# Kernel optimization log

Hardware: AMD Instinct MI355X
Metric: run time of the kernel (lower is better)

Reference implementation:

```python
import jax, jax.numpy as jnp
import numpy as np
from jax import lax

N = 25600      # total nodes = G * T
E = 204800     # edges (before self loops)
IN_CH = 6
HID = 64
HEADS = 4
G = 512        # graphs per batch
T = 50         # sequence length (node_time in [0, T))
OUT = 30       # prediction_horizon * 3
NEG_SLOPE = 0.2
BN_EPS = 1e-5


def _gat(x, src, dst, W, a_src, a_dst, b, heads, outc):
    # PyG GATConv (concat=True): h = x W reshaped to (N, H, C)
    n = x.shape[0]
    h = (x @ W).reshape(n, heads, outc)
    # edge scores: leaky_relu(a_src . h_src + a_dst . h_dst), softmax over incoming edges of dst
    e = jax.nn.leaky_relu((h * a_src).sum(-1)[src] + (h * a_dst).sum(-1)[dst], NEG_SLOPE)  # (E, H)
    m = jax.ops.segment_max(e, dst, num_segments=n)
    ex = jnp.exp(e - m[dst])
    denom = jax.ops.segment_sum(ex, dst, num_segments=n)
    alpha = ex / denom[dst]
    out = jax.ops.segment_sum(alpha[:, :, None] * h[src], dst, num_segments=n)  # (N, H, C)
    return out.reshape(n, heads * outc) + b


def _bn_eval(x, g, b):
    # BatchNorm in eval with running_mean=0, running_var=1
    return g * (x * (1.0 / np.float32(np.sqrt(1.0 + BN_EPS)))) + b


def setup_inputs() -> dict:
    ks = jax.random.split(jax.random.key(0), 16)
    s = 0.1
    d = {}
    d["x"] = jax.random.normal(ks[0], (N, IN_CH), jnp.float32)
    d["edge_index"] = jax.random.randint(ks[1], (2, E), 0, N)
    idx = jnp.arange(N)
    d["batch"] = idx // T       # each graph has exactly T nodes
    d["node_time"] = idx % T
    d["W1"] = jax.random.normal(ks[2], (IN_CH, HEADS * HID), jnp.float32) * s
    d["att_src1"] = jax.random.normal(ks[3], (HEADS, HID), jnp.float32) * s
    d["att_dst1"] = jax.random.normal(ks[4], (HEADS, HID), jnp.float32) * s
    d["b1"] = jnp.zeros((HEADS * HID,), jnp.float32)
    d["g1"] = jnp.ones((HEADS * HID,), jnp.float32)
    d["be1"] = jnp.zeros((HEADS * HID,), jnp.float32)
    d["W2"] = jax.random.normal(ks[5], (HEADS * HID, HID), jnp.float32) * s
    d["att_src2"] = jax.random.normal(ks[6], (1, HID), jnp.float32) * s
    d["att_dst2"] = jax.random.normal(ks[7], (1, HID), jnp.float32) * s
    d["b2"] = jnp.zeros((HID,), jnp.float32)
    d["g2"] = jnp.ones((HID,), jnp.float32)
    d["be2"] = jnp.zeros((HID,), jnp.float32)
    d["Wih"] = jax.random.normal(ks[8], (4 * HID, HID), jnp.float32) * s
    d["Whh"] = jax.random.normal(ks[9], (4 * HID, HID), jnp.float32) * s
    d["bih"] = jnp.zeros((4 * HID,), jnp.float32)
    d["bhh"] = jnp.zeros((4 * HID,), jnp.float32)
    d["Wfc"] = jax.random.normal(ks[10], (HID, OUT), jnp.float32) * s
    d["bfc"] = jnp.zeros((OUT,), jnp.float32)
    return d


def reference(x, edge_index, batch, node_time, W1, att_src1, att_dst1, b1, g1, be1,
              W2, att_src2, att_dst2, b2, g2, be2, Wih, Whh, bih, bhh, Wfc, bfc):
    loops = jnp.arange(N)
    src = jnp.concatenate([edge_index[0], loops])  # GATConv adds self loops
    dst = jnp.concatenate([edge_index[1], loops])
    h = jax.nn.elu(_bn_eval(_gat(x, src, dst, W1, att_src1, att_dst1, b1, HEADS, HID), g1, be1))
    h = jax.nn.elu(_bn_eval(_gat(h, src, dst, W2, att_src2, att_dst2, b2, 1, HID), g2, be2))
    # vectorized replacement of the per-node python scatter loop
    x_seq = jnp.zeros((G, T, HID), h.dtype).at[batch, node_time].set(h)

    def step(carry, xt):
        hh, cc = carry
        gates = xt @ Wih.T + bih + hh @ Whh.T + bhh
        i, f, gg, o = jnp.split(gates, 4, axis=-1)
        cc = jax.nn.sigmoid(f) * cc + jax.nn.sigmoid(i) * jnp.tanh(gg)
        hh = jax.nn.sigmoid(o) * jnp.tanh(cc)
        return (hh, cc), None

    init = (jnp.zeros((G, HID), h.dtype), jnp.zeros((G, HID), h.dtype))
    (hn, _), _ = lax.scan(step, init, x_seq.transpose(1, 0, 2))  # scan over time
    return hn @ Wfc + bfc  # (G, 30)
```

## Files before the change

### kernel.cpp

```cpp
#include <hip/hip_runtime.h>

#define N_NODES 25600
#define N_EDGES 204800
#define EE (N_EDGES + N_NODES)
#define IN_CH 6
#define HID 64
#define HEADS 4
#define G_GRAPHS 512
#define T_STEPS 50
#define OUT_DIM 30
#define NEG_SLOPE 0.2f
#define BN_INV 0.9999950000374997f

__device__ __forceinline__ float lrelu_(float x){ return x > 0.f ? x : NEG_SLOPE * x; }
__device__ __forceinline__ float elu_(float x){ return x > 0.f ? x : __expf(x) - 1.f; }
__device__ __forceinline__ float sigmoid_(float x){
    return __builtin_amdgcn_rcpf(1.f + __expf(-x));
}
__device__ __forceinline__ float tanh_(float x){
    return 1.f - 2.f * __builtin_amdgcn_rcpf(1.f + __expf(2.f * x));
}

__global__ void count_k(const int* __restrict__ ei, int* __restrict__ counts){
    int e = blockIdx.x * 256 + threadIdx.x;
    if (e >= EE) return;
    int dst = (e < N_EDGES) ? ei[N_EDGES + e] : (e - N_EDGES);
    atomicAdd(&counts[dst], 1);
}

__global__ void scan_k(const int* __restrict__ counts, int* __restrict__ row_ptr,
                       int* __restrict__ cursor){
    __shared__ int part[1024];
    int t = threadIdx.x;
    const int CH = N_NODES / 1024;
    int base = t * CH;
    int s = 0;
    for (int i = 0; i < CH; i++) s += counts[base + i];
    part[t] = s;
    __syncthreads();
    for (int off = 1; off < 1024; off <<= 1){
        int v = (t >= off) ? part[t - off] : 0;
        __syncthreads();
        part[t] += v;
        __syncthreads();
    }
    int run = (t > 0) ? part[t - 1] : 0;
    for (int i = 0; i < CH; i++){
        int cv = counts[base + i];
        row_ptr[base + i] = run;
        cursor[base + i]  = run;
        run += cv;
    }
    if (t == 1023) row_ptr[N_NODES] = run;
}

__global__ void scatter_k(const int* __restrict__ ei, int* __restrict__ cursor,
                          int* __restrict__ ssrc){
    int e = blockIdx.x * 256 + threadIdx.x;
    if (e >= EE) return;
    int src, dst;
    if (e < N_EDGES){ src = ei[e]; dst = ei[N_EDGES + e]; }
    else            { src = dst = e - N_EDGES; }
    int pos = atomicAdd(&cursor[dst], 1);
    ssrc[pos] = src;
}

__global__ void ns_k(const float* __restrict__ x, const float* __restrict__ W1,
                     const float* __restrict__ asw, const float* __restrict__ adw,
                     float* __restrict__ as1, float* __restrict__ ad1){
    __shared__ float waS[IN_CH * 4], waD[IN_CH * 4];
    int t = threadIdx.x;
    if (t < 48){
        int k = t >> 3, h = (t >> 1) & 3, which = t & 1;
        const float* a = which ? adw : asw;
        float s = 0.f;
        #pragma unroll
        for (int c = 0; c < 64; c++) s += W1[k * 256 + h * 64 + c] * a[h * 64 + c];
        (which ? waD : waS)[k * 4 + h] = s;
    }
    __syncthreads();
    int n = blockIdx.x * 256 + t;
    float xv[IN_CH];
    #pragma unroll
    for (int k = 0; k < IN_CH; k++) xv[k] = x[n * IN_CH + k];
    float sv[4] = {0.f, 0.f, 0.f, 0.f}, dv[4] = {0.f, 0.f, 0.f, 0.f};
    #pragma unroll
    for (int k = 0; k < IN_CH; k++){
        #pragma unroll
        for (int h = 0; h < 4; h++){
            sv[h] += xv[k] * waS[k * 4 + h];
            dv[h] += xv[k] * waD[k * 4 + h];
        }
    }
    *(float4*)&as1[n * 4] = make_float4(sv[0], sv[1], sv[2], sv[3]);
    *(float4*)&ad1[n * 4] = make_float4(dv[0], dv[1], dv[2], dv[3]);
}

__global__ void gat1_aggx(const float* __restrict__ x, const float* __restrict__ as1,
                          const float* __restrict__ ad1, const int* __restrict__ row_ptr,
                          const int* __restrict__ ssrc, const float* __restrict__ W1,
                          const float* __restrict__ b1, const float* __restrict__ g1,
                          const float* __restrict__ be1, float* __restrict__ h1_act){
    __shared__ float w1s[IN_CH * 256];
    int tid = threadIdx.x;
    for (int i = tid; i < IN_CH * 256; i += 256) w1s[i] = W1[i];
    __syncthreads();
    int wv = tid >> 6, lane = tid & 63;
    int n = blockIdx.x * 4 + wv;
    int s0 = row_ptr[n], s1 = row_ptr[n + 1];
    float4 adn = *(const float4*)&ad1[n * 4];
    float xs0[IN_CH] = {}, xs1[IN_CH] = {}, xs2[IN_CH] = {}, xs3[IN_CH] = {};
    float d0 = 0.f, d1 = 0.f, d2 = 0.f, d3 = 0.f;
    for (int j = s0; j < s1; j++){
        int s = ssrc[j];
        float4 as = *(const float4*)&as1[s * 4];
        float e0 = __expf(lrelu_(as.x + adn.x));
        float e1 = __expf(lrelu_(as.y + adn.y));
        float e2 = __expf(lrelu_(as.z + adn.z));
        float e3 = __expf(lrelu_(as.w + adn.w));
        d0 += e0; d1 += e1; d2 += e2; d3 += e3;
        const float2* xp = (const float2*)(x + (size_t)s * IN_CH);
        float2 xa = xp[0], xb = xp[1], xc = xp[2];
        float xv[IN_CH] = {xa.x, xa.y, xb.x, xb.y, xc.x, xc.y};
        #pragma unroll
        for (int k = 0; k < IN_CH; k++){
            xs0[k] += e0 * xv[k];
            xs1[k] += e1 * xv[k];
            xs2[k] += e2 * xv[k];
            xs3[k] += e3 * xv[k];
        }
    }
    float r0 = 1.f / d0, r1 = 1.f / d1, r2 = 1.f / d2, r3 = 1.f / d3;
    #pragma unroll
    for (int h = 0; h < 4; h++){
        const float* xsh = (h == 0) ? xs0 : (h == 1) ? xs1 : (h == 2) ? xs2 : xs3;
        float rh = (h == 0) ? r0 : (h == 1) ? r1 : (h == 2) ? r2 : r3;
        int col = h * 64 + lane;
        float acc = 0.f;
        #pragma unroll
        for (int k = 0; k < IN_CH; k++) acc += xsh[k] * w1s[k * 256 + col];
        float v = acc * rh + b1[col];
        v = g1[col] * (v * BN_INV) + be1[col];
        h1_act[(size_t)n * 256 + col] = elu_(v);
    }
}

#define TM 64
#define KT 32
#define APAD 4
__global__ __launch_bounds__(256) void gat2_tr(const float* __restrict__ h1_act,
                        const float* __restrict__ W2,
                        const float* __restrict__ asw, const float* __restrict__ adw,
                        float* __restrict__ h2_pre, float* __restrict__ as2,
                        float* __restrict__ ad2){
    __shared__ float As[TM][KT + APAD];
    __shared__ float Bs[KT][64];
    int tx = threadIdx.x;
    int rg = tx >> 4;
    int cg = tx & 15;
    int r0 = rg * 4, c0 = cg * 4;
    int rowBase = blockIdx.x * TM;
    float acc[4][4] = {};
    for (int k0 = 0; k0 < 256; k0 += KT){
        #pragma unroll
        for (int it = 0; it < 2; it++){
            int i = tx + it * 256;
            int row = i >> 3;
            int c4  = (i & 7) * 4;
            *(float4*)&As[row][c4] =
                *(const float4*)(h1_act + (size_t)(rowBase + row) * 256 + k0 + c4);
        }
        #pragma unroll
        for (int it = 0; it < 2; it++){
            int i = tx + it * 256;
            int row = i >> 4;
            int c4  = (i & 15) * 4;
            *(float4*)&Bs[row][c4] = *(const float4*)(W2 + (size_t)(k0 + row) * 64 + c4);
        }
        __syncthreads();
        #pragma unroll
        for (int kq = 0; kq < KT; kq += 4){
            float4 b0 = *(float4*)&Bs[kq + 0][c0];
            float4 b1v = *(float4*)&Bs[kq + 1][c0];
            float4 b2v = *(float4*)&Bs[kq + 2][c0];
            float4 b3 = *(float4*)&Bs[kq + 3][c0];
            #pragma unroll
            for (int i = 0; i < 4; i++){
                float4 a = *(float4*)&As[r0 + i][kq];
                acc[i][0] += a.x * b0.x + a.y * b1v.x + a.z * b2v.x + a.w * b3.x;
                acc[i][1] += a.x * b0.y + a.y * b1v.y + a.z * b2v.y + a.w * b3.y;
                acc[i][2] += a.x * b0.z + a.y * b1v.z + a.z * b2v.z + a.w * b3.z;
                acc[i][3] += a.x * b0.w + a.y * b1v.w + a.z * b2v.w + a.w * b3.w;
            }
        }
        __syncthreads();
    }
    float aw0 = asw[c0], aw1 = asw[c0+1], aw2 = asw[c0+2], aw3 = asw[c0+3];
    float dw0 = adw[c0], dw1 = adw[c0+1], dw2 = adw[c0+2], dw3 = adw[c0+3];
    #pragma unroll
    for (int i = 0; i < 4; i++){
        int row = rowBase + r0 + i;
        *(float4*)(h2_pre + (size_t)row * 64 + c0) =
            make_float4(acc[i][0], acc[i][1], acc[i][2], acc[i][3]);
        float sA = acc[i][0]*aw0 + acc[i][1]*aw1 + acc[i][2]*aw2 + acc[i][3]*aw3;
        float sD = acc[i][0]*dw0 + acc[i][1]*dw1 + acc[i][2]*dw2 + acc[i][3]*dw3;
        #pragma unroll
        for (int off = 8; off; off >>= 1){
            sA += __shfl_xor(sA, off);
            sD += __shfl_xor(sD, off);
        }
        if (cg == 0){ as2[row] = sA; ad2[row] = sD; }
    }
}

__global__ __launch_bounds__(256, 2) void gat2_aggp(const float* __restrict__ h2_pre,
        const float* __restrict__ as2, const float* __restrict__ ad2,
        const int* __restrict__ row_ptr, const int* __restrict__ ssrc,
        const float* __restrict__ b2, const float* __restrict__ g2,
        const float* __restrict__ be2,
        const int* __restrict__ batch, const int* __restrict__ ntime,
        const float* __restrict__ Wih, const float* __restrict__ bih,
        const float* __restrict__ bhh, float* __restrict__ gx){
    __shared__ float vsh[16][64];
    __shared__ int posb[16];
    int tx = threadIdx.x, wv = tx >> 6, lane = tx & 63;
    float4 wih[16];
    const float4* Wr = (const float4*)(Wih + tx * 64);
    #pragma unroll
    for (int k = 0; k < 16; k++) wih[k] = Wr[k];
    float bsum = bih[tx] + bhh[tx];
    int nbase = blockIdx.x * 16;
    for (int q = 0; q < 4; q++){
        int n = nbase + wv * 4 + q;
        int s0 = row_ptr[n], s1 = row_ptr[n + 1];
        float adn = ad2[n];
        float denom = 0.f, acc = 0.f;
        int j = s0;
        for (; j + 4 <= s1; j += 4){
            int sa = ssrc[j], sb = ssrc[j + 1], sc = ssrc[j + 2], sd = ssrc[j + 3];
            float ea = __expf(lrelu_(as2[sa] + adn));
            float eb = __expf(lrelu_(as2[sb] + adn));
            float ec = __expf(lrelu_(as2[sc] + adn));
            float ed = __expf(lrelu_(as2[sd] + adn));
            float ha = h2_pre[(size_t)sa * 64 + lane];
            float hb = h2_pre[(size_t)sb * 64 + lane];
            float hc = h2_pre[(size_t)sc * 64 + lane];
            float hd = h2_pre[(size_t)sd * 64 + lane];
            denom += (ea + eb) + (ec + ed);
            acc += ea * ha + eb * hb + ec * hc + ed * hd;
        }
        for (; j < s1; j++){
            int s = ssrc[j];
            float e = __expf(lrelu_(as2[s] + adn));
            denom += e;
            acc += e * h2_pre[(size_t)s * 64 + lane];
        }
        float v = acc / denom + b2[lane];
        v = g2[lane] * (v * BN_INV) + be2[lane];
        vsh[wv * 4 + q][lane] = elu_(v);
        if (lane == 0) posb[wv * 4 + q] = batch[n] * T_STEPS + ntime[n];
    }
    __syncthreads();
    #pragma unroll
    for (int q = 0; q < 16; q++){
        const float4* vp = (const float4*)vsh[q];
        float a0 = 0.f, a1 = 0.f, a2 = 0.f, a3 = 0.f;
        #pragma unroll
        for (int k = 0; k < 16; k++){
            float4 vv = vp[k];
            float4 ww = wih[k];
            a0 += ww.x * vv.x;
            a1 += ww.y * vv.y;
            a2 += ww.z * vv.z;
            a3 += ww.w * vv.w;
        }
        gx[(size_t)posb[q] * 256 + tx] = bsum + (a0 + a1) + (a2 + a3);
    }
}

__global__ __launch_bounds__(256, 2) void lstm_k(const float* __restrict__ gx,
        const float* __restrict__ Whh,
        const float* __restrict__ Wfc, const float* __restrict__ bfc,
        float* __restrict__ out){
    int g = blockIdx.x;
    int j = threadIdx.x;
    int wv = j >> 6, lane = j & 63;
    __shared__ float gates[2][256];
    __shared__ float hb[4][2][64];
    float4 whh[16];
    const float4* Hr = (const float4*)(Whh + j * 64);
    #pragma unroll
    for (int k = 0; k < 16; k++) whh[k] = Hr[k];
    float c = 0.f;
    hb[wv][0][lane] = 0.f;
    const float* gxg = gx + (size_t)g * T_STEPS * 256;
    float gxv = gxg[j];
    float hn = 0.f;
    for (int t = 0; t < T_STEPS; t++){
        float gx_next = (t + 1 < T_STEPS) ? gxg[(t + 1) * 256 + j] : 0.f;
        int buf = t & 1;
        const float4* hp = (const float4*)hb[wv][buf];
        float a0 = gxv, a1 = 0.f, a2 = 0.f, a3 = 0.f;
        #pragma unroll
        for (int k = 0; k < 16; k++){
            float4 hv = hp[k];
            float4 wvv = whh[k];
            a0 += wvv.x * hv.x;
            a1 += wvv.y * hv.y;
            a2 += wvv.z * hv.z;
            a3 += wvv.w * hv.w;
        }
        gates[buf][j] = (a0 + a1) + (a2 + a3);
        __syncthreads();
        float iv = gates[buf][lane];
        float fv = gates[buf][64 + lane];
        float gv = gates[buf][128 + lane];
        float ov = gates[buf][192 + lane];
        c = sigmoid_(fv) * c + sigmoid_(iv) * tanh_(gv);
        hn = sigmoid_(ov) * tanh_(c);
        hb[wv][buf ^ 1][lane] = hn;
        gxv = gx_next;
    }
    if (wv == 0) gates[0][lane] = hn;
    __syncthreads();
    if (j < OUT_DIM){
        float acc = bfc[j];
        #pragma unroll
        for (int k = 0; k < 64; k++) acc += gates[0][k] * Wfc[k * OUT_DIM + j];
        out[g * OUT_DIM + j] = acc;
    }
}

extern "C" void kernel_launch(void* const* d_in, const int* in_sizes, int n_in,
                              void* d_out, int out_size, void* d_ws, size_t ws_size,
                              hipStream_t stream){
    const float* x    = (const float*)d_in[0];
    const int*   ei   = (const int*)  d_in[1];
    const int*   batch= (const int*)  d_in[2];
    const int*   ntime= (const int*)  d_in[3];
    const float* W1   = (const float*)d_in[4];
    const float* as1w = (const float*)d_in[5];
    const float* ad1w = (const float*)d_in[6];
    const float* b1   = (const float*)d_in[7];
    const float* g1   = (const float*)d_in[8];
    const float* be1  = (const float*)d_in[9];
    const float* W2   = (const float*)d_in[10];
    const float* as2w = (const float*)d_in[11];
    const float* ad2w = (const float*)d_in[12];
    const float* b2   = (const float*)d_in[13];
    const float* g2   = (const float*)d_in[14];
    const float* be2  = (const float*)d_in[15];
    const float* Wih  = (const float*)d_in[16];
    const float* Whh  = (const float*)d_in[17];
    const float* bih  = (const float*)d_in[18];
    const float* bhh  = (const float*)d_in[19];
    const float* Wfc  = (const float*)d_in[20];
    const float* bfc  = (const float*)d_in[21];
    float* out = (float*)d_out;

    char* w = (char*)d_ws;
    auto alloc = [&](size_t bytes)->char*{
        char* p = w;
        w += (bytes + 255) & ~size_t(255);
        return p;
    };
    float* h1_act = (float*)alloc((size_t)N_NODES * 256 * 4);
    float* gx     = (float*)alloc((size_t)N_NODES * 256 * 4);
    float* h2_pre = (float*)alloc((size_t)N_NODES * 64 * 4);
    float* as1    = (float*)alloc((size_t)N_NODES * 4 * 4);
    float* ad1    = (float*)alloc((size_t)N_NODES * 4 * 4);
    float* as2    = (float*)alloc((size_t)N_NODES * 4);
    float* ad2    = (float*)alloc((size_t)N_NODES * 4);
    int* counts   = (int*)alloc((size_t)N_NODES * 4);
    int* row_ptr  = (int*)alloc((size_t)(N_NODES + 1) * 4);
    int* cursor   = (int*)alloc((size_t)N_NODES * 4);
    int* ssrc     = (int*)alloc((size_t)EE * 4);

    hipMemsetAsync(counts, 0, (size_t)N_NODES * 4, stream);
    count_k  <<<(EE + 255) / 256, 256, 0, stream>>>(ei, counts);
    scan_k   <<<1, 1024, 0, stream>>>(counts, row_ptr, cursor);
    scatter_k<<<(EE + 255) / 256, 256, 0, stream>>>(ei, cursor, ssrc);
    ns_k     <<<N_NODES / 256, 256, 0, stream>>>(x, W1, as1w, ad1w, as1, ad1);
    gat1_aggx<<<N_NODES / 4, 256, 0, stream>>>(x, as1, ad1, row_ptr, ssrc, W1, b1, g1, be1, h1_act);
    gat2_tr  <<<N_NODES / TM, 256, 0, stream>>>(h1_act, W2, as2w, ad2w, h2_pre, as2, ad2);
    gat2_aggp<<<N_NODES / 16, 256, 0, stream>>>(h2_pre, as2, ad2, row_ptr, ssrc, b2, g2, be2,
                                                batch, ntime, Wih, bih, bhh, gx);
    lstm_k   <<<G_GRAPHS, 256, 0, stream>>>(gx, Whh, Wfc, bfc, out);
}
```

Baseline: 291.4 us.

## Use lane broadcasts for input projection and LSTM recurrence, two graphs per block

Adds a kernel that transposes Wih so the gate-projection epilogue in gat2_aggp streams coalesced weight rows and broadcasts node features via readlane, instead of holding 64 weights per thread in registers. The LSTM kernel now runs two graphs per 512-thread block, broadcasts the hidden state across lanes with readlane instead of a shared-memory buffer, and reloads Whh rows from memory each step rather than keeping them in registers. The aim is lower register pressure and higher occupancy. The cost is an extra launch and more global/L1 traffic for weights. Within each wavefront all 64 hidden values are available, so the lane broadcast is correct.

```diff
diff --git a/kernel.cpp b/kernel.cpp
--- a/kernel.cpp
+++ b/kernel.cpp
@@ -20,6 +20,9 @@
 __device__ __forceinline__ float tanh_(float x){
     return 1.f - 2.f * __builtin_amdgcn_rcpf(1.f + __expf(2.f * x));
 }
+__device__ __forceinline__ float bcast_(float v, int l){
+    return __int_as_float(__builtin_amdgcn_readlane(__float_as_int(v), l));
+}
 
 __global__ void count_k(const int* __restrict__ ei, int* __restrict__ counts){
     int e = blockIdx.x * 256 + threadIdx.x;
@@ -63,6 +66,21 @@
     else            { src = dst = e - N_EDGES; }
     int pos = atomicAdd(&cursor[dst], 1);
     ssrc[pos] = src;
+}
+
+__global__ void twih_k(const float* __restrict__ Wih, float* __restrict__ WihT){
+    __shared__ float tile[64][65];
+    int t = threadIdx.x;
+    int jb = blockIdx.x * 64;
+    for (int i = t; i < 64 * 64; i += 256){
+        int j = i >> 6, k = i & 63;
+        tile[k][j] = Wih[(size_t)(jb + j) * 64 + k];
+    }
+    __syncthreads();
+    for (int i = t; i < 64 * 64; i += 256){
+        int k = i >> 6, j = i & 63;
+        WihT[(size_t)k * 256 + jb + j] = tile[k][j];
+    }
 }
 
 __global__ void ns_k(const float* __restrict__ x, const float* __restrict__ W1,
@@ -219,16 +237,11 @@
         const float* __restrict__ b2, const float* __restrict__ g2,
         const float* __restrict__ be2,
         const int* __restrict__ batch, const int* __restrict__ ntime,
-        const float* __restrict__ Wih, const float* __restrict__ bih,
+        const float* __restrict__ WihT, const float* __restrict__ bih,
         const float* __restrict__ bhh, float* __restrict__ gx){
     __shared__ float vsh[16][64];
     __shared__ int posb[16];
     int tx = threadIdx.x, wv = tx >> 6, lane = tx & 63;
-    float4 wih[16];
-    const float4* Wr = (const float4*)(Wih + tx * 64);
-    #pragma unroll
-    for (int k = 0; k < 16; k++) wih[k] = Wr[k];
-    float bsum = bih[tx] + bhh[tx];
     int nbase = blockIdx.x * 16;
     for (int q = 0; q < 4; q++){
         int n = nbase + wv * 4 + q;
@@ -261,73 +274,65 @@
         if (lane == 0) posb[wv * 4 + q] = batch[n] * T_STEPS + ntime[n];
     }
     __syncthreads();
-    #pragma unroll
-    for (int q = 0; q < 16; q++){
-        const float4* vp = (const float4*)vsh[q];
-        float a0 = 0.f, a1 = 0.f, a2 = 0.f, a3 = 0.f;
-        #pragma unroll
-        for (int k = 0; k < 16; k++){
-            float4 vv = vp[k];
-            float4 ww = wih[k];
-            a0 += ww.x * vv.x;
-            a1 += ww.y * vv.y;
-            a2 += ww.z * vv.z;
-            a3 += ww.w * vv.w;
-        }
-        gx[(size_t)posb[q] * 256 + tx] = bsum + (a0 + a1) + (a2 + a3);
-    }
-}
-
-__global__ __launch_bounds__(256, 2) void lstm_k(const float* __restrict__ gx,
+    float vq[16];
+    #pragma unroll
+    for (int q = 0; q < 16; q++) vq[q] = vsh[q][lane];
+    float bsum = bih[tx] + bhh[tx];
+    float acc[16];
+    #pragma unroll
+    for (int q = 0; q < 16; q++) acc[q] = bsum;
+    #pragma unroll 4
+    for (int k = 0; k < 64; k++){
+        float wk = WihT[(size_t)k * 256 + tx];
+        #pragma unroll
+        for (int q = 0; q < 16; q++)
+            acc[q] += wk * bcast_(vq[q], k);
+    }
+    #pragma unroll
+    for (int q = 0; q < 16; q++)
+        gx[(size_t)posb[q] * 256 + tx] = acc[q];
+}
+
+__global__ __launch_bounds__(512, 2) void lstm_k(const float* __restrict__ gx,
         const float* __restrict__ Whh,
         const float* __restrict__ Wfc, const float* __restrict__ bfc,
         float* __restrict__ out){
-    int g = blockIdx.x;
-    int j = threadIdx.x;
-    int wv = j >> 6, lane = j & 63;
-    __shared__ float gates[2][256];
-    __shared__ float hb[4][2][64];
-    float4 whh[16];
-    const float4* Hr = (const float4*)(Whh + j * 64);
-    #pragma unroll
-    for (int k = 0; k < 16; k++) whh[k] = Hr[k];
-    float c = 0.f;
-    hb[wv][0][lane] = 0.f;
-    const float* gxg = gx + (size_t)g * T_STEPS * 256;
-    float gxv = gxg[j];
-    float hn = 0.f;
+    int g0 = blockIdx.x * 2;
+    int t0 = threadIdx.x;
+    int gr = t0 >> 8;
+    int j  = t0 & 255;
+    int lane = t0 & 63;
+    __shared__ float gates[2][2][256];
+    const float4* Wr = (const float4*)(Whh + (size_t)j * 64);
+    const float* gxg = gx + (size_t)(g0 + gr) * T_STEPS * 256 + j;
+    float c = 0.f, hn = 0.f;
     for (int t = 0; t < T_STEPS; t++){
-        float gx_next = (t + 1 < T_STEPS) ? gxg[(t + 1) * 256 + j] : 0.f;
         int buf = t & 1;
-        const float4* hp = (const float4*)hb[wv][buf];
-        float a0 = gxv, a1 = 0.f, a2 = 0.f, a3 = 0.f;
+        float a0 = gxg[t * 256], a1 = 0.f, a2 = 0.f, a3 = 0.f;
         #pragma unroll
         for (int k = 0; k < 16; k++){
-            float4 hv = hp[k];
-            float4 wvv = whh[k];
-            a0 += wvv.x * hv.x;
-            a1 += wvv.y * hv.y;
-            a2 += wvv.z * hv.z;
-            a3 += wvv.w * hv.w;
-        }
-        gates[buf][j] = (a0 + a1) + (a2 + a3);
-        __syncthreads();
-        float iv = gates[buf][lane];
-        float fv = gates[buf][64 + lane];
-        float gv = gates[buf][128 + lane];
-        float ov = gates[buf][192 + lane];
+            float4 wv = Wr[k];
+            a0 += wv.x * bcast_(hn, 4 * k + 0);
+            a1 += wv.y * bcast_(hn, 4 * k + 1);
+            a2 += wv.z * bcast_(hn, 4 * k + 2);
+            a3 += wv.w * bcast_(hn, 4 * k + 3);
+        }
+        gates[gr][buf][j] = (a0 + a1) + (a2 + a3);
+        __syncthreads();
+        float iv = gates[gr][buf][lane];
+        float fv = gates[gr][buf][64 + lane];
+        float gv = gates[gr][buf][128 + lane];
+        float ov = gates[gr][buf][192 + lane];
         c = sigmoid_(fv) * c + sigmoid_(iv) * tanh_(gv);
         hn = sigmoid_(ov) * tanh_(c);
-        hb[wv][buf ^ 1][lane] = hn;
-        gxv = gx_next;
-    }
-    if (wv == 0) gates[0][lane] = hn;
+    }
+    if (j < 64) gates[gr][0][j] = hn;
     __syncthreads();
     if (j < OUT_DIM){
         float acc = bfc[j];
         #pragma unroll
-        for (int k = 0; k < 64; k++) acc += gates[0][k] * Wfc[k * OUT_DIM + j];
-        out[g * OUT_DIM + j] = acc;
+        for (int k = 0; k < 64; k++) acc += gates[gr][0][k] * Wfc[k * OUT_DIM + j];
+        out[(g0 + gr) * OUT_DIM + j] = acc;
     }
 }
 
@@ -367,6 +372,7 @@
     float* h1_act = (float*)alloc((size_t)N_NODES * 256 * 4);
     float* gx     = (float*)alloc((size_t)N_NODES * 256 * 4);
     float* h2_pre = (float*)alloc((size_t)N_NODES * 64 * 4);
+    float* WihT   = (float*)alloc((size_t)64 * 256 * 4);
     float* as1    = (float*)alloc((size_t)N_NODES * 4 * 4);
     float* ad1    = (float*)alloc((size_t)N_NODES * 4 * 4);
     float* as2    = (float*)alloc((size_t)N_NODES * 4);
@@ -380,10 +386,11 @@
     count_k  <<<(EE + 255) / 256, 256, 0, stream>>>(ei, counts);
     scan_k   <<<1, 1024, 0, stream>>>(counts, row_ptr, cursor);
     scatter_k<<<(EE + 255) / 256, 256, 0, stream>>>(ei, cursor, ssrc);
+    twih_k   <<<4, 256, 0, stream>>>(Wih, WihT);
     ns_k     <<<N_NODES / 256, 256, 0, stream>>>(x, W1, as1w, ad1w, as1, ad1);
     gat1_aggx<<<N_NODES / 4, 256, 0, stream>>>(x, as1, ad1, row_ptr, ssrc, W1, b1, g1, be1, h1_act);
     gat2_tr  <<<N_NODES / TM, 256, 0, stream>>>(h1_act, W2, as2w, ad2w, h2_pre, as2, ad2);
     gat2_aggp<<<N_NODES / 16, 256, 0, stream>>>(h2_pre, as2, ad2, row_ptr, ssrc, b2, g2, be2,
-                                                batch, ntime, Wih, bih, bhh, gx);
-    lstm_k   <<<G_GRAPHS, 256, 0, stream>>>(gx, Whh, Wfc, bfc, out);
-}
+                                                batch, ntime, WihT, bih, bhh, gx);
+    lstm_k   <<<G_GRAPHS / 2, 512, 0, stream>>>(gx, Whh, Wfc, bfc, out);
+}
```

Result: no change. 296.6 us (+1.8%).
